# Kernel optimization log

Measured on AMD Instinct MI355X. Metric: run time of the kernel, lower is better.

The kernel has to match this reference:

```python
import jax, jax.numpy as jnp
import numpy as np

DIM = 768
NUM_HEADS = 8
HEAD_DIM = DIM // NUM_HEADS


def setup_inputs() -> dict:
    key = jax.random.key(0)
    k1, k2, k3, k4, k5 = jax.random.split(key, 5)
    B, C, H, W = 16, DIM, 32, 32
    x = jax.random.normal(k1, (B, C, H, W), dtype=jnp.float32)
    # Conv2d 1x1 weights expressed as [out_ch, in_ch] matrices
    w_qkv = jax.random.normal(k2, (3 * C, C), dtype=jnp.float32) * (C ** -0.5)
    b_qkv = jax.random.normal(k3, (3 * C,), dtype=jnp.float32) * 0.02
    w_proj = jax.random.normal(k4, (C, C), dtype=jnp.float32) * (C ** -0.5)
    b_proj = jax.random.normal(k5, (C,), dtype=jnp.float32) * 0.02
    return {"x": x, "w_qkv": w_qkv, "b_qkv": b_qkv, "w_proj": w_proj, "b_proj": b_proj}


def reference(x, w_qkv, b_qkv, w_proj, b_proj):
    B, C, H, W = x.shape
    N = H * W
    nh, hd = NUM_HEADS, C // NUM_HEADS
    xf = x.astype(jnp.float32).reshape(B, C, N)  # bcn
    # 1x1 conv == channel matmul
    qkv = jnp.einsum('oc,bcn->bon', w_qkv, xf) + b_qkv[None, :, None]
    qkv = qkv.reshape(B, 3, nh, hd, N)
    q, k, v = qkv[:, 0], qkv[:, 1], qkv[:, 2]  # [B, nh, hd, N]
    s = hd ** -0.25  # scale split between q and k as in the original
    attn = jnp.einsum('bhdn,bhdm->bhnm', q * s, k * s)  # [B, nh, N, N]
    attn = attn - jax.lax.stop_gradient(jnp.max(attn, axis=-1, keepdims=True))
    attn = jnp.clip(attn, -88.0, 88.0)
    attn = jax.nn.softmax(attn, axis=-1)
    # dropout is identity in eval mode
    out = jnp.einsum('bhnm,bhdm->bhdn', attn, v)  # [B, nh, hd, N]
    out = out.reshape(B, C, N)
    out = jnp.einsum('oc,bcn->bon', w_proj, out) + b_proj[None, :, None]
    return out.reshape(B, C, H, W).astype(x.dtype)
```

## Files before the change

kernel.cpp:

```cpp
#include <hip/hip_runtime.h>
#include <stdint.h>

typedef __attribute__((ext_vector_type(4))) float f32x4;
typedef __attribute__((ext_vector_type(16))) float f32x16;
typedef __attribute__((ext_vector_type(8))) short bf16x8;

#define SQKV 0.38372606f

__device__ __forceinline__ unsigned short f2bf(float f) {
  union { float f; unsigned u; } v; v.f = f;
  unsigned r = v.u + 0x7FFFu + ((v.u >> 16) & 1u);
  return (unsigned short)(r >> 16);
}

__device__ __forceinline__ unsigned cvt_pk_bf16(float a, float b) {
  unsigned r;
  asm volatile("v_cvt_pk_bf16_f32 %0, %1, %2" : "=v"(r) : "v"(a), "v"(b));
  return r;
}
__device__ __forceinline__ void permswap(unsigned &a, unsigned &b) {
  asm volatile("v_permlane32_swap_b32 %0, %1" : "+v"(a), "+v"(b));
}

__global__ __launch_bounds__(256) void k_convert(const float* __restrict__ src,
                                                 unsigned short* __restrict__ dst,
                                                 int n4) {
  int i = blockIdx.x * 256 + threadIdx.x;
  if (i >= n4) return;
  float4 v = reinterpret_cast<const float4*>(src)[i];
  ushort4 o;
  o.x = f2bf(v.x); o.y = f2bf(v.y); o.z = f2bf(v.z); o.w = f2bf(v.w);
  reinterpret_cast<ushort4*>(dst)[i] = o;
}

__global__ __launch_bounds__(256) void k_transpose(const float* __restrict__ x,
                                                   unsigned short* __restrict__ xT) {
  __shared__ float tile[32][33];
  const int t = threadIdx.x;
  const int j = t & 31, i0 = t >> 5;
  const int n0 = blockIdx.x * 32, c0 = blockIdx.y * 32, b = blockIdx.z;
  const float* src = x + ((size_t)b * 768 + c0) * 1024 + n0;
#pragma unroll
  for (int q = 0; q < 4; ++q)
    tile[i0 + q * 8][j] = src[(size_t)(i0 + q * 8) * 1024 + j];
  __syncthreads();
  unsigned short* dst = xT + ((size_t)b * 1024 + n0) * 768 + c0;
#pragma unroll
  for (int q = 0; q < 4; ++q)
    dst[(size_t)(i0 + q * 8) * 768 + j] = f2bf(tile[j][i0 + q * 8]);
}

__global__ __launch_bounds__(256, 2) void k_gemm_qkv(
    const unsigned short* __restrict__ A,
    const unsigned short* __restrict__ Bx,
    const float* __restrict__ bias,
    unsigned short* __restrict__ qT,
    unsigned short* __restrict__ kT,
    unsigned short* __restrict__ vO) {
  __shared__ unsigned short As[128][40];
  __shared__ unsigned short Bs[128][40];
  const int t = threadIdx.x;
  const int b = blockIdx.y;
  const int tm = blockIdx.x >> 3, tn = blockIdx.x & 7;
  const int lane = t & 63, w = t >> 6, wr = w >> 1, wc = w & 1;

  const int ar0 = t >> 2, ac0 = (t & 3) << 3;
  const int ar1 = ar0 + 64;
  const unsigned short* aptr0 = A + (size_t)(tm * 128 + ar0) * 768 + ac0;
  const unsigned short* aptr1 = A + (size_t)(tm * 128 + ar1) * 768 + ac0;
  const unsigned short* bptr0 = Bx + (size_t)b * 1024 * 768 + (size_t)(tn * 128 + ar0) * 768 + ac0;
  const unsigned short* bptr1 = Bx + (size_t)b * 1024 * 768 + (size_t)(tn * 128 + ar1) * 768 + ac0;

  uint4 sa0 = *(const uint4*)aptr0;
  uint4 sa1 = *(const uint4*)aptr1;
  uint4 sb0 = *(const uint4*)bptr0;
  uint4 sb1 = *(const uint4*)bptr1;

  uint4* const wA0 = reinterpret_cast<uint4*>(&As[ar0][ac0]);
  uint4* const wA1 = reinterpret_cast<uint4*>(&As[ar1][ac0]);
  uint4* const wB0 = reinterpret_cast<uint4*>(&Bs[ar0][ac0]);
  uint4* const wB1 = reinterpret_cast<uint4*>(&Bs[ar1][ac0]);

  f32x4 acc[4][4];
#pragma unroll
  for (int mi = 0; mi < 4; ++mi)
#pragma unroll
    for (int ni = 0; ni < 4; ++ni) acc[mi][ni] = (f32x4)0.0f;

  const unsigned short* rA[4];
  const unsigned short* rB[4];
#pragma unroll
  for (int mi = 0; mi < 4; ++mi)
    rA[mi] = &As[wr * 64 + mi * 16 + (lane & 15)][(lane >> 4) << 3];
#pragma unroll
  for (int ni = 0; ni < 4; ++ni)
    rB[ni] = &Bs[wc * 64 + ni * 16 + (lane & 15)][(lane >> 4) << 3];

  for (int kt = 0; kt < 24; ++kt) {
    __syncthreads();
    *wA0 = sa0; *wA1 = sa1; *wB0 = sb0; *wB1 = sb1;
    __syncthreads();
    if (kt < 23) {
      aptr0 += 32; aptr1 += 32; bptr0 += 32; bptr1 += 32;
      sa0 = *(const uint4*)aptr0;
      sa1 = *(const uint4*)aptr1;
      sb0 = *(const uint4*)bptr0;
      sb1 = *(const uint4*)bptr1;
    }
    bf16x8 af[4], bfr[4];
#pragma unroll
    for (int mi = 0; mi < 4; ++mi) af[mi] = *reinterpret_cast<const bf16x8*>(rA[mi]);
#pragma unroll
    for (int ni = 0; ni < 4; ++ni) bfr[ni] = *reinterpret_cast<const bf16x8*>(rB[ni]);
#pragma unroll
    for (int mi = 0; mi < 4; ++mi)
#pragma unroll
      for (int ni = 0; ni < 4; ++ni)
        acc[mi][ni] = __builtin_amdgcn_mfma_f32_16x16x32_bf16(af[mi], bfr[ni], acc[mi][ni], 0, 0, 0);
  }

#pragma unroll
  for (int mi = 0; mi < 4; ++mi) {
    const int o0 = tm * 128 + wr * 64 + mi * 16 + ((lane >> 4) << 2);
    const float4 bb = *reinterpret_cast<const float4*>(bias + o0);
    const float sc = (o0 < 1536) ? SQKV : 1.0f;
    const int om = o0 % 768;
    const int hh = om / 96;
    const int d0 = om % 96;
    const int region = o0 / 768;
    const size_t bh = (size_t)(b * 8 + hh);
#pragma unroll
    for (int ni = 0; ni < 4; ++ni) {
      const int nn = tn * 128 + wc * 64 + ni * 16 + (lane & 15);
      ushort4 st;
      st.x = f2bf((acc[mi][ni][0] + bb.x) * sc);
      st.y = f2bf((acc[mi][ni][1] + bb.y) * sc);
      st.z = f2bf((acc[mi][ni][2] + bb.z) * sc);
      st.w = f2bf((acc[mi][ni][3] + bb.w) * sc);
      if (region == 0) {
        *reinterpret_cast<ushort4*>(qT + (bh * 1024 + nn) * 96 + d0) = st;
      } else if (region == 1) {
        *reinterpret_cast<ushort4*>(kT + (bh * 1024 + nn) * 96 + d0) = st;
      } else {
        unsigned short* vp = vO + (bh * 96 + d0) * 1024 + nn;
        vp[0] = st.x; vp[1024] = st.y; vp[2048] = st.z; vp[3072] = st.w;
      }
    }
  }
}

__global__ __launch_bounds__(512, 2) void k_attn2(
    const unsigned short* __restrict__ qT,
    const unsigned short* __restrict__ kT,
    const unsigned short* __restrict__ vO,
    unsigned short* __restrict__ attoutT) {
  __shared__ unsigned short Ks[64][104];
  __shared__ unsigned short Vs[96][72];
  __shared__ float redbuf[8][32];

  const int t = threadIdx.x, lane = t & 63, wv = t >> 6;
  const int r31 = lane & 31, h = lane >> 5;
  const int sw = (blockIdx.x & 7) * 64 + (blockIdx.x >> 3);
  const int bh = sw >> 2, qt = sw & 3;
  const int b = bh >> 3, hh = bh & 7;
  const int n0 = qt * 256 + wv * 32;

  bf16x8 Qf[6];
  {
    const unsigned short* qrow = qT + ((size_t)bh * 1024 + n0 + r31) * 96 + h * 8;
#pragma unroll
    for (int ks = 0; ks < 6; ++ks)
      Qf[ks] = *reinterpret_cast<const bf16x8*>(qrow + ks * 16);
  }

  const unsigned short* gptr[3];
  unsigned short* lptr[3];
  int gstep[3];
#pragma unroll
  for (int i = 0; i < 3; ++i) {
    const int cc = t + i * 512;
    if (cc < 768) {
      const int row = cc / 12, col = (cc % 12) * 8;
      gptr[i] = kT + ((size_t)bh * 1024 + row) * 96 + col;
      lptr[i] = &Ks[row][col];
      gstep[i] = 64 * 96;
    } else {
      const int cv = cc - 768;
      const int d = cv >> 3, col = (cv & 7) * 8;
      gptr[i] = vO + ((size_t)bh * 96 + d) * 1024 + col;
      lptr[i] = &Vs[d][col];
      gstep[i] = 64;
    }
  }
  uint4 rg[3];
#pragma unroll
  for (int i = 0; i < 3; ++i) rg[i] = *reinterpret_cast<const uint4*>(gptr[i]);

  f32x16 oac[3];
#pragma unroll
  for (int dt = 0; dt < 3; ++dt) oac[dt] = (f32x16)0.0f;
  float run_m = -3.0e38f, run_l = 0.0f;

  for (int mt = 0; mt < 16; ++mt) {
    __syncthreads();
#pragma unroll
    for (int i = 0; i < 3; ++i) *reinterpret_cast<uint4*>(lptr[i]) = rg[i];
    __syncthreads();
    if (mt < 15) {
#pragma unroll
      for (int i = 0; i < 3; ++i) {
        gptr[i] += gstep[i];
        rg[i] = *reinterpret_cast<const uint4*>(gptr[i]);
      }
    }

    f32x16 sa = (f32x16)0.0f, sb = (f32x16)0.0f;
    __builtin_amdgcn_s_setprio(1);
#pragma unroll
    for (int ks = 0; ks < 6; ++ks) {
      const bf16x8 k0 = *reinterpret_cast<const bf16x8*>(&Ks[r31][ks * 16 + h * 8]);
      const bf16x8 k1 = *reinterpret_cast<const bf16x8*>(&Ks[32 + r31][ks * 16 + h * 8]);
      sa = __builtin_amdgcn_mfma_f32_32x32x16_bf16(k0, Qf[ks], sa, 0, 0, 0);
      sb = __builtin_amdgcn_mfma_f32_32x32x16_bf16(k1, Qf[ks], sb, 0, 0, 0);
    }
    __builtin_amdgcn_s_setprio(0);

    float m4a = fmaxf(sa[0], sa[1]), m4b = fmaxf(sa[2], sa[3]);
    float m4c = fmaxf(sb[0], sb[1]), m4d = fmaxf(sb[2], sb[3]);
#pragma unroll
    for (int i = 4; i < 16; i += 4) {
      m4a = fmaxf(m4a, fmaxf(sa[i], sa[i + 1]));
      m4b = fmaxf(m4b, fmaxf(sa[i + 2], sa[i + 3]));
      m4c = fmaxf(m4c, fmaxf(sb[i], sb[i + 1]));
      m4d = fmaxf(m4d, fmaxf(sb[i + 2], sb[i + 3]));
    }
    float tmax = fmaxf(fmaxf(m4a, m4b), fmaxf(m4c, m4d));
    tmax = fmaxf(tmax, __shfl_xor(tmax, 32));

    if (__any(tmax - run_m > 8.0f)) {
      const float nm = fmaxf(run_m, tmax);
      const float alpha = __builtin_amdgcn_exp2f(run_m - nm);
      run_m = nm;
      run_l *= alpha;
      if (lane < 32) redbuf[wv][lane] = alpha;
      f32x4 a4[4];
#pragma unroll
      for (int q = 0; q < 4; ++q)
        a4[q] = *reinterpret_cast<const f32x4*>(&redbuf[wv][q * 8 + h * 4]);
#pragma unroll
      for (int dt = 0; dt < 3; ++dt)
#pragma unroll
        for (int q = 0; q < 4; ++q)
#pragma unroll
          for (int j = 0; j < 4; ++j)
            oac[dt][q * 4 + j] *= a4[q][j];
    }

    float t0 = 0.f, t1 = 0.f, t2 = 0.f, t3 = 0.f;
#pragma unroll
    for (int i = 0; i < 16; i += 4) {
      sa[i]     = __builtin_amdgcn_exp2f(sa[i] - run_m);     t0 += sa[i];
      sa[i + 1] = __builtin_amdgcn_exp2f(sa[i + 1] - run_m); t1 += sa[i + 1];
      sa[i + 2] = __builtin_amdgcn_exp2f(sa[i + 2] - run_m); t2 += sa[i + 2];
      sa[i + 3] = __builtin_amdgcn_exp2f(sa[i + 3] - run_m); t3 += sa[i + 3];
    }
#pragma unroll
    for (int i = 0; i < 16; i += 4) {
      sb[i]     = __builtin_amdgcn_exp2f(sb[i] - run_m);     t0 += sb[i];
      sb[i + 1] = __builtin_amdgcn_exp2f(sb[i + 1] - run_m); t1 += sb[i + 1];
      sb[i + 2] = __builtin_amdgcn_exp2f(sb[i + 2] - run_m); t2 += sb[i + 2];
      sb[i + 3] = __builtin_amdgcn_exp2f(sb[i + 3] - run_m); t3 += sb[i + 3];
    }
    float ts = (t0 + t1) + (t2 + t3);
    ts += __shfl_xor(ts, 32);
    run_l += ts;

    union { bf16x8 v; unsigned u[4]; } pf;
    __builtin_amdgcn_s_setprio(1);
#pragma unroll
    for (int kst = 0; kst < 4; ++kst) {
      const f32x16& s = (kst < 2) ? sa : sb;
      const int base = (kst & 1) * 8;
      unsigned X = cvt_pk_bf16(s[base + 0], s[base + 1]);
      unsigned Y = cvt_pk_bf16(s[base + 2], s[base + 3]);
      unsigned Z = cvt_pk_bf16(s[base + 4], s[base + 5]);
      unsigned W = cvt_pk_bf16(s[base + 6], s[base + 7]);
      permswap(X, Z);
      permswap(Y, W);
      pf.u[0] = X; pf.u[1] = Y; pf.u[2] = Z; pf.u[3] = W;
#pragma unroll
      for (int dt = 0; dt < 3; ++dt) {
        const bf16x8 vf = *reinterpret_cast<const bf16x8*>(&Vs[dt * 32 + r31][kst * 16 + h * 8]);
        oac[dt] = __builtin_amdgcn_mfma_f32_32x32x16_bf16(pf.v, vf, oac[dt], 0, 0, 0);
      }
    }
    __builtin_amdgcn_s_setprio(0);
  }

  if (lane < 32) redbuf[wv][lane] = 1.0f / run_l;
  f32x4 i4[4];
#pragma unroll
  for (int q = 0; q < 4; ++q)
    i4[q] = *reinterpret_cast<const f32x4*>(&redbuf[wv][q * 8 + h * 4]);
  unsigned short* obase = attoutT + ((size_t)b * 1024 + n0) * 768 + hh * 96;
#pragma unroll
  for (int dt = 0; dt < 3; ++dt)
#pragma unroll
    for (int q = 0; q < 4; ++q)
#pragma unroll
      for (int j = 0; j < 4; ++j) {
        const int np = q * 8 + h * 4 + j;
        obase[(size_t)np * 768 + dt * 32 + r31] = f2bf(oac[dt][q * 4 + j] * i4[q][j]);
      }
}

__global__ __launch_bounds__(256, 2) void k_gemm_proj(
    const unsigned short* __restrict__ Aat,
    const unsigned short* __restrict__ Bw,
    const float* __restrict__ bias,
    float* __restrict__ out) {
  __shared__ unsigned short As[128][40];
  __shared__ unsigned short Bs[128][40];
  const int t = threadIdx.x;
  const int b = blockIdx.y;
  const int tm = blockIdx.x / 6, tn = blockIdx.x % 6;
  const int lane = t & 63, w = t >> 6, wr = w >> 1, wc = w & 1;

  const int ar0 = t >> 2, ac0 = (t & 3) << 3;
  const int ar1 = ar0 + 64;
  const unsigned short* aptr0 = Aat + (size_t)b * 1024 * 768 + (size_t)(tm * 128 + ar0) * 768 + ac0;
  const unsigned short* aptr1 = Aat + (size_t)b * 1024 * 768 + (size_t)(tm * 128 + ar1) * 768 + ac0;
  const unsigned short* bptr0 = Bw + (size_t)(tn * 128 + ar0) * 768 + ac0;
  const unsigned short* bptr1 = Bw + (size_t)(tn * 128 + ar1) * 768 + ac0;

  uint4 sa0 = *(const uint4*)aptr0;
  uint4 sa1 = *(const uint4*)aptr1;
  uint4 sb0 = *(const uint4*)bptr0;
  uint4 sb1 = *(const uint4*)bptr1;

  uint4* const wA0 = reinterpret_cast<uint4*>(&As[ar0][ac0]);
  uint4* const wA1 = reinterpret_cast<uint4*>(&As[ar1][ac0]);
  uint4* const wB0 = reinterpret_cast<uint4*>(&Bs[ar0][ac0]);
  uint4* const wB1 = reinterpret_cast<uint4*>(&Bs[ar1][ac0]);

  f32x4 acc[4][4];
#pragma unroll
  for (int mi = 0; mi < 4; ++mi)
#pragma unroll
    for (int ni = 0; ni < 4; ++ni) acc[mi][ni] = (f32x4)0.0f;

  const unsigned short* rA[4];
  const unsigned short* rB[4];
#pragma unroll
  for (int mi = 0; mi < 4; ++mi)
    rA[mi] = &As[wr * 64 + mi * 16 + (lane & 15)][(lane >> 4) << 3];
#pragma unroll
  for (int ni = 0; ni < 4; ++ni)
    rB[ni] = &Bs[wc * 64 + ni * 16 + (lane & 15)][(lane >> 4) << 3];

  for (int kt = 0; kt < 24; ++kt) {
    __syncthreads();
    *wA0 = sa0; *wA1 = sa1; *wB0 = sb0; *wB1 = sb1;
    __syncthreads();
    if (kt < 23) {
      aptr0 += 32; aptr1 += 32; bptr0 += 32; bptr1 += 32;
      sa0 = *(const uint4*)aptr0;
      sa1 = *(const uint4*)aptr1;
      sb0 = *(const uint4*)bptr0;
      sb1 = *(const uint4*)bptr1;
    }
    bf16x8 af[4], bfr[4];
#pragma unroll
    for (int mi = 0; mi < 4; ++mi) af[mi] = *reinterpret_cast<const bf16x8*>(rA[mi]);
#pragma unroll
    for (int ni = 0; ni < 4; ++ni) bfr[ni] = *reinterpret_cast<const bf16x8*>(rB[ni]);
#pragma unroll
    for (int mi = 0; mi < 4; ++mi)
#pragma unroll
      for (int ni = 0; ni < 4; ++ni)
        acc[mi][ni] = __builtin_amdgcn_mfma_f32_16x16x32_bf16(af[mi], bfr[ni], acc[mi][ni], 0, 0, 0);
  }

#pragma unroll
  for (int mi = 0; mi < 4; ++mi) {
    const int n0 = tm * 128 + wr * 64 + mi * 16 + ((lane >> 4) << 2);
#pragma unroll
    for (int ni = 0; ni < 4; ++ni) {
      const int o = tn * 128 + wc * 64 + ni * 16 + (lane & 15);
      const float bo = bias[o];
      float4 vv;
      vv.x = acc[mi][ni][0] + bo;
      vv.y = acc[mi][ni][1] + bo;
      vv.z = acc[mi][ni][2] + bo;
      vv.w = acc[mi][ni][3] + bo;
      *reinterpret_cast<float4*>(out + ((size_t)b * 768 + o) * 1024 + n0) = vv;
    }
  }
}

extern "C" void kernel_launch(void* const* d_in, const int* in_sizes, int n_in,
                              void* d_out, int out_size, void* d_ws, size_t ws_size,
                              hipStream_t stream) {
  const float* x = (const float*)d_in[0];
  const float* w_qkv = (const float*)d_in[1];
  const float* b_qkv = (const float*)d_in[2];
  const float* w_proj = (const float*)d_in[3];
  const float* b_proj = (const float*)d_in[4];
  float* out = (float*)d_out;

  unsigned short* ws = (unsigned short*)d_ws;
  unsigned short* wqkv_bf = ws;
  unsigned short* wproj_bf = wqkv_bf + 2304 * 768;
  unsigned short* xT = wproj_bf + 768 * 768;
  unsigned short* qT = xT + (size_t)16 * 1024 * 768;
  unsigned short* kT = qT + (size_t)16 * 8 * 1024 * 96;
  unsigned short* vO = kT + (size_t)16 * 8 * 1024 * 96;
  unsigned short* attoutT = xT;

  k_convert<<<(2304 * 768 / 4 + 255) / 256, 256, 0, stream>>>(w_qkv, wqkv_bf, 2304 * 768 / 4);
  k_convert<<<(768 * 768 / 4 + 255) / 256, 256, 0, stream>>>(w_proj, wproj_bf, 768 * 768 / 4);
  k_transpose<<<dim3(32, 24, 16), 256, 0, stream>>>(x, xT);
  k_gemm_qkv<<<dim3(144, 16), 256, 0, stream>>>(wqkv_bf, xT, b_qkv, qT, kT, vO);
  k_attn2<<<512, 512, 0, stream>>>(qT, kT, vO, attoutT);
  k_gemm_proj<<<dim3(48, 16), 256, 0, stream>>>(attoutT, wproj_bf, b_proj, out);
}
```

Before: 241.8 us.

## Use direct global-to-LDS loads in GEMMs and shrink attention blocks

Both GEMM kernels replace register-staged prefetch with global_load_lds direct-to-LDS copies into unpadded tiles and raise the occupancy hint to 4 blocks per CU. The attention kernel is halved to 256 threads covering 128 query rows, with twice as many blocks. The intent is to cut register pressure and VGPR-to-LDS store instructions and to improve occupancy and load balance. In exchange, the GEMMs lose load/compute overlap, the unpadded LDS layout may cause bank conflicts, and attention re-reads K/V twice as often.

```diff
diff --git a/kernel.cpp b/kernel.cpp
--- a/kernel.cpp
+++ b/kernel.cpp
@@ -20,6 +20,12 @@
 }
 __device__ __forceinline__ void permswap(unsigned &a, unsigned &b) {
   asm volatile("v_permlane32_swap_b32 %0, %1" : "+v"(a), "+v"(b));
+}
+
+__device__ __forceinline__ void glds16(const unsigned short* g, unsigned short* l) {
+  __builtin_amdgcn_global_load_lds(
+      (const __attribute__((address_space(1))) void*)g,
+      (__attribute__((address_space(3))) void*)l, 16, 0, 0);
 }
 
 __global__ __launch_bounds__(256) void k_convert(const float* __restrict__ src,
@@ -50,36 +56,30 @@
     dst[(size_t)(i0 + q * 8) * 768 + j] = f2bf(tile[j][i0 + q * 8]);
 }
 
-__global__ __launch_bounds__(256, 2) void k_gemm_qkv(
+__global__ __launch_bounds__(256, 4) void k_gemm_qkv(
     const unsigned short* __restrict__ A,
     const unsigned short* __restrict__ Bx,
     const float* __restrict__ bias,
     unsigned short* __restrict__ qT,
     unsigned short* __restrict__ kT,
     unsigned short* __restrict__ vO) {
-  __shared__ unsigned short As[128][40];
-  __shared__ unsigned short Bs[128][40];
+  __shared__ unsigned short As[128 * 32];
+  __shared__ unsigned short Bs[128 * 32];
   const int t = threadIdx.x;
   const int b = blockIdx.y;
   const int tm = blockIdx.x >> 3, tn = blockIdx.x & 7;
   const int lane = t & 63, w = t >> 6, wr = w >> 1, wc = w & 1;
 
-  const int ar0 = t >> 2, ac0 = (t & 3) << 3;
-  const int ar1 = ar0 + 64;
-  const unsigned short* aptr0 = A + (size_t)(tm * 128 + ar0) * 768 + ac0;
-  const unsigned short* aptr1 = A + (size_t)(tm * 128 + ar1) * 768 + ac0;
-  const unsigned short* bptr0 = Bx + (size_t)b * 1024 * 768 + (size_t)(tn * 128 + ar0) * 768 + ac0;
-  const unsigned short* bptr1 = Bx + (size_t)b * 1024 * 768 + (size_t)(tn * 128 + ar1) * 768 + ac0;
-
-  uint4 sa0 = *(const uint4*)aptr0;
-  uint4 sa1 = *(const uint4*)aptr1;
-  uint4 sb0 = *(const uint4*)bptr0;
-  uint4 sb1 = *(const uint4*)bptr1;
-
-  uint4* const wA0 = reinterpret_cast<uint4*>(&As[ar0][ac0]);
-  uint4* const wA1 = reinterpret_cast<uint4*>(&As[ar1][ac0]);
-  uint4* const wB0 = reinterpret_cast<uint4*>(&Bs[ar0][ac0]);
-  uint4* const wB1 = reinterpret_cast<uint4*>(&Bs[ar1][ac0]);
+  const int srow = 16 * w + (lane >> 2);
+  const int scol = (lane & 3) * 8;
+  const unsigned short* aptr0 = A + (size_t)(tm * 128 + srow) * 768 + scol;
+  const unsigned short* aptr1 = aptr0 + (size_t)64 * 768;
+  const unsigned short* bptr0 = Bx + (size_t)b * 1024 * 768 + (size_t)(tn * 128 + srow) * 768 + scol;
+  const unsigned short* bptr1 = bptr0 + (size_t)64 * 768;
+  unsigned short* const lA0 = As + 512 * w;
+  unsigned short* const lA1 = As + 2048 + 512 * w;
+  unsigned short* const lB0 = Bs + 512 * w;
+  unsigned short* const lB1 = Bs + 2048 + 512 * w;
 
   f32x4 acc[4][4];
 #pragma unroll
@@ -91,22 +91,20 @@
   const unsigned short* rB[4];
 #pragma unroll
   for (int mi = 0; mi < 4; ++mi)
-    rA[mi] = &As[wr * 64 + mi * 16 + (lane & 15)][(lane >> 4) << 3];
+    rA[mi] = As + (wr * 64 + mi * 16 + (lane & 15)) * 32 + ((lane >> 4) << 3);
 #pragma unroll
   for (int ni = 0; ni < 4; ++ni)
-    rB[ni] = &Bs[wc * 64 + ni * 16 + (lane & 15)][(lane >> 4) << 3];
+    rB[ni] = Bs + (wc * 64 + ni * 16 + (lane & 15)) * 32 + ((lane >> 4) << 3);
 
   for (int kt = 0; kt < 24; ++kt) {
     __syncthreads();
-    *wA0 = sa0; *wA1 = sa1; *wB0 = sb0; *wB1 = sb1;
-    __syncthreads();
-    if (kt < 23) {
-      aptr0 += 32; aptr1 += 32; bptr0 += 32; bptr1 += 32;
-      sa0 = *(const uint4*)aptr0;
-      sa1 = *(const uint4*)aptr1;
-      sb0 = *(const uint4*)bptr0;
-      sb1 = *(const uint4*)bptr1;
-    }
+    glds16(aptr0, lA0);
+    glds16(aptr1, lA1);
+    glds16(bptr0, lB0);
+    glds16(bptr1, lB1);
+    aptr0 += 32; aptr1 += 32; bptr0 += 32; bptr1 += 32;
+    __syncthreads();
+
     bf16x8 af[4], bfr[4];
 #pragma unroll
     for (int mi = 0; mi < 4; ++mi) af[mi] = *reinterpret_cast<const bf16x8*>(rA[mi]);
@@ -149,21 +147,21 @@
   }
 }
 
-__global__ __launch_bounds__(512, 2) void k_attn2(
+__global__ __launch_bounds__(256, 2) void k_attn2(
     const unsigned short* __restrict__ qT,
     const unsigned short* __restrict__ kT,
     const unsigned short* __restrict__ vO,
     unsigned short* __restrict__ attoutT) {
   __shared__ unsigned short Ks[64][104];
   __shared__ unsigned short Vs[96][72];
-  __shared__ float redbuf[8][32];
+  __shared__ float redbuf[4][32];
 
   const int t = threadIdx.x, lane = t & 63, wv = t >> 6;
   const int r31 = lane & 31, h = lane >> 5;
-  const int sw = (blockIdx.x & 7) * 64 + (blockIdx.x >> 3);
-  const int bh = sw >> 2, qt = sw & 3;
+  const int sw = (blockIdx.x & 7) * 128 + (blockIdx.x >> 3);
+  const int bh = sw >> 3, qt = sw & 7;
   const int b = bh >> 3, hh = bh & 7;
-  const int n0 = qt * 256 + wv * 32;
+  const int n0 = qt * 128 + wv * 32;
 
   bf16x8 Qf[6];
   {
@@ -173,28 +171,25 @@
       Qf[ks] = *reinterpret_cast<const bf16x8*>(qrow + ks * 16);
   }
 
-  const unsigned short* gptr[3];
-  unsigned short* lptr[3];
-  int gstep[3];
-#pragma unroll
-  for (int i = 0; i < 3; ++i) {
-    const int cc = t + i * 512;
-    if (cc < 768) {
+  const unsigned short* gptr[6];
+  unsigned short* lptr[6];
+#pragma unroll
+  for (int i = 0; i < 6; ++i) {
+    if (i < 3) {
+      const int cc = t + i * 256;
       const int row = cc / 12, col = (cc % 12) * 8;
       gptr[i] = kT + ((size_t)bh * 1024 + row) * 96 + col;
       lptr[i] = &Ks[row][col];
-      gstep[i] = 64 * 96;
     } else {
-      const int cv = cc - 768;
+      const int cv = t + (i - 3) * 256;
       const int d = cv >> 3, col = (cv & 7) * 8;
       gptr[i] = vO + ((size_t)bh * 96 + d) * 1024 + col;
       lptr[i] = &Vs[d][col];
-      gstep[i] = 64;
-    }
-  }
-  uint4 rg[3];
-#pragma unroll
-  for (int i = 0; i < 3; ++i) rg[i] = *reinterpret_cast<const uint4*>(gptr[i]);
+    }
+  }
+  uint4 rg[6];
+#pragma unroll
+  for (int i = 0; i < 6; ++i) rg[i] = *reinterpret_cast<const uint4*>(gptr[i]);
 
   f32x16 oac[3];
 #pragma unroll
@@ -204,12 +199,12 @@
   for (int mt = 0; mt < 16; ++mt) {
     __syncthreads();
 #pragma unroll
-    for (int i = 0; i < 3; ++i) *reinterpret_cast<uint4*>(lptr[i]) = rg[i];
+    for (int i = 0; i < 6; ++i) *reinterpret_cast<uint4*>(lptr[i]) = rg[i];
     __syncthreads();
     if (mt < 15) {
 #pragma unroll
-      for (int i = 0; i < 3; ++i) {
-        gptr[i] += gstep[i];
+      for (int i = 0; i < 6; ++i) {
+        gptr[i] += (i < 3) ? 64 * 96 : 64;
         rg[i] = *reinterpret_cast<const uint4*>(gptr[i]);
       }
     }
@@ -314,34 +309,28 @@
       }
 }
 
-__global__ __launch_bounds__(256, 2) void k_gemm_proj(
+__global__ __launch_bounds__(256, 4) void k_gemm_proj(
     const unsigned short* __restrict__ Aat,
     const unsigned short* __restrict__ Bw,
     const float* __restrict__ bias,
     float* __restrict__ out) {
-  __shared__ unsigned short As[128][40];
-  __shared__ unsigned short Bs[128][40];
+  __shared__ unsigned short As[128 * 32];
+  __shared__ unsigned short Bs[128 * 32];
   const int t = threadIdx.x;
   const int b = blockIdx.y;
   const int tm = blockIdx.x / 6, tn = blockIdx.x % 6;
   const int lane = t & 63, w = t >> 6, wr = w >> 1, wc = w & 1;
 
-  const int ar0 = t >> 2, ac0 = (t & 3) << 3;
-  const int ar1 = ar0 + 64;
-  const unsigned short* aptr0 = Aat + (size_t)b * 1024 * 768 + (size_t)(tm * 128 + ar0) * 768 + ac0;
-  const unsigned short* aptr1 = Aat + (size_t)b * 1024 * 768 + (size_t)(tm * 128 + ar1) * 768 + ac0;
-  const unsigned short* bptr0 = Bw + (size_t)(tn * 128 + ar0) * 768 + ac0;
-  const unsigned short* bptr1 = Bw + (size_t)(tn * 128 + ar1) * 768 + ac0;
-
-  uint4 sa0 = *(const uint4*)aptr0;
-  uint4 sa1 = *(const uint4*)aptr1;
-  uint4 sb0 = *(const uint4*)bptr0;
-  uint4 sb1 = *(const uint4*)bptr1;
-
-  uint4* const wA0 = reinterpret_cast<uint4*>(&As[ar0][ac0]);
-  uint4* const wA1 = reinterpret_cast<uint4*>(&As[ar1][ac0]);
-  uint4* const wB0 = reinterpret_cast<uint4*>(&Bs[ar0][ac0]);
-  uint4* const wB1 = reinterpret_cast<uint4*>(&Bs[ar1][ac0]);
+  const int srow = 16 * w + (lane >> 2);
+  const int scol = (lane & 3) * 8;
+  const unsigned short* aptr0 = Aat + (size_t)b * 1024 * 768 + (size_t)(tm * 128 + srow) * 768 + scol;
+  const unsigned short* aptr1 = aptr0 + (size_t)64 * 768;
+  const unsigned short* bptr0 = Bw + (size_t)(tn * 128 + srow) * 768 + scol;
+  const unsigned short* bptr1 = bptr0 + (size_t)64 * 768;
+  unsigned short* const lA0 = As + 512 * w;
+  unsigned short* const lA1 = As + 2048 + 512 * w;
+  unsigned short* const lB0 = Bs + 512 * w;
+  unsigned short* const lB1 = Bs + 2048 + 512 * w;
 
   f32x4 acc[4][4];
 #pragma unroll
@@ -353,22 +342,20 @@
   const unsigned short* rB[4];
 #pragma unroll
   for (int mi = 0; mi < 4; ++mi)
-    rA[mi] = &As[wr * 64 + mi * 16 + (lane & 15)][(lane >> 4) << 3];
+    rA[mi] = As + (wr * 64 + mi * 16 + (lane & 15)) * 32 + ((lane >> 4) << 3);
 #pragma unroll
   for (int ni = 0; ni < 4; ++ni)
-    rB[ni] = &Bs[wc * 64 + ni * 16 + (lane & 15)][(lane >> 4) << 3];
+    rB[ni] = Bs + (wc * 64 + ni * 16 + (lane & 15)) * 32 + ((lane >> 4) << 3);
 
   for (int kt = 0; kt < 24; ++kt) {
     __syncthreads();
-    *wA0 = sa0; *wA1 = sa1; *wB0 = sb0; *wB1 = sb1;
-    __syncthreads();
-    if (kt < 23) {
-      aptr0 += 32; aptr1 += 32; bptr0 += 32; bptr1 += 32;
-      sa0 = *(const uint4*)aptr0;
-      sa1 = *(const uint4*)aptr1;
-      sb0 = *(const uint4*)bptr0;
-      sb1 = *(const uint4*)bptr1;
-    }
+    glds16(aptr0, lA0);
+    glds16(aptr1, lA1);
+    glds16(bptr0, lB0);
+    glds16(bptr1, lB1);
+    aptr0 += 32; aptr1 += 32; bptr0 += 32; bptr1 += 32;
+    __syncthreads();
+
     bf16x8 af[4], bfr[4];
 #pragma unroll
     for (int mi = 0; mi < 4; ++mi) af[mi] = *reinterpret_cast<const bf16x8*>(rA[mi]);
@@ -421,6 +408,6 @@
   k_convert<<<(768 * 768 / 4 + 255) / 256, 256, 0, stream>>>(w_proj, wproj_bf, 768 * 768 / 4);
   k_transpose<<<dim3(32, 24, 16), 256, 0, stream>>>(x, xT);
   k_gemm_qkv<<<dim3(144, 16), 256, 0, stream>>>(wqkv_bf, xT, b_qkv, qT, kT, vO);
-  k_attn2<<<512, 512, 0, stream>>>(qT, kT, vO, attoutT);
+  k_attn2<<<1024, 256, 0, stream>>>(qT, kT, vO, attoutT);
   k_gemm_proj<<<dim3(48, 16), 256, 0, stream>>>(attoutT, wproj_bf, b_proj, out);
 }
```

After: 263.0 us. 8.8% more time.
